# Kernel optimization log

Measured on AMD Instinct MI355X. Metric: run time of the kernel, lower is better.

Reference implementation:

```python
import jax, jax.numpy as jnp
import numpy as np

N_CLASSES = 18

def setup_inputs() -> dict:
    key = jax.random.key(0)
    k1, k2 = jax.random.split(key)
    B = 2_000_000
    output = jax.random.normal(k1, (B, N_CLASSES), dtype=jnp.float32)
    labels_soft = jax.random.uniform(k2, (B, N_CLASSES), dtype=jnp.float32)
    return {"output": output, "labels_soft": labels_soft}

def reference(output, labels_soft):
    # Original: sum over classes of mean_b( CE(output, cls) * labels_soft[:, cls] )
    # = mean over batch of sum_c( -log_softmax(output)[b, c] * labels_soft[b, c] )
    logp = jax.nn.log_softmax(output, axis=-1)          # [B, C]
    per_row = -jnp.sum(logp * labels_soft, axis=-1)     # [B]
    return jnp.mean(per_row)
```

## Files before the change

### kernel.cpp

```cpp
#include <hip/hip_runtime.h>

#define NCLS 18
#define TILE_ROWS 256
#define TILE_F2 (TILE_ROWS * NCLS / 2)
#define GRID_A 2048

__global__ __launch_bounds__(256) void ce_soft_kernel(
    const float2* __restrict__ logits2,
    const float2* __restrict__ labels2,
    float* __restrict__ partials,
    int B)
{
    __shared__ float2 sX[TILE_F2];
    __shared__ float2 sL[TILE_F2];

    const int t = threadIdx.x;
    const int nTiles = (B + TILE_ROWS - 1) / TILE_ROWS;

    float acc = 0.0f;
    for (int tile = blockIdx.x; tile < nTiles; tile += gridDim.x) {
        const int rowBase = tile * TILE_ROWS;
        const int rows = min(TILE_ROWS, B - rowBase);
        const int n2 = rows * (NCLS / 2);
        const size_t g2 = (size_t)rowBase * (NCLS / 2);

        for (int g = t; g < n2; g += 256) {
            sX[g] = logits2[g2 + g];
            sL[g] = labels2[g2 + g];
        }
        __syncthreads();

        if (t < rows) {
            const float2* xr = &sX[t * (NCLS / 2)];
            const float2* lr = &sL[t * (NCLS / 2)];
            float x[NCLS];
            #pragma unroll
            for (int j = 0; j < NCLS / 2; ++j) {
                float2 v = xr[j];
                x[2 * j] = v.x; x[2 * j + 1] = v.y;
            }
            float m = x[0];
            #pragma unroll
            for (int c = 1; c < NCLS; ++c) m = fmaxf(m, x[c]);

            float se = 0.0f, dot = 0.0f, sl = 0.0f;
            #pragma unroll
            for (int j = 0; j < NCLS / 2; ++j) {
                float2 w = lr[j];
                se += __expf(x[2 * j] - m) + __expf(x[2 * j + 1] - m);
                dot = fmaf(w.x, x[2 * j], dot);
                dot = fmaf(w.y, x[2 * j + 1], dot);
                sl += w.x + w.y;
            }
            float lse = m + __logf(se);
            acc = fmaf(sl, lse, acc - dot);
        }
        __syncthreads();
    }

    #pragma unroll
    for (int off = 32; off > 0; off >>= 1)
        acc += __shfl_down(acc, off, 64);

    __shared__ float wave_sums[4];
    const int lane = t & 63;
    const int wid  = t >> 6;
    if (lane == 0) wave_sums[wid] = acc;
    __syncthreads();
    if (t == 0)
        partials[blockIdx.x] = wave_sums[0] + wave_sums[1] + wave_sums[2] + wave_sums[3];
}

__global__ __launch_bounds__(256) void ce_reduce_kernel(
    const float* __restrict__ partials, float* __restrict__ out, int n, float invB)
{
    float acc = 0.0f;
    for (int i = threadIdx.x; i < n; i += 256) acc += partials[i];

    #pragma unroll
    for (int off = 32; off > 0; off >>= 1)
        acc += __shfl_down(acc, off, 64);

    __shared__ float wave_sums[4];
    const int lane = threadIdx.x & 63;
    const int wid  = threadIdx.x >> 6;
    if (lane == 0) wave_sums[wid] = acc;
    __syncthreads();
    if (threadIdx.x == 0)
        out[0] = (wave_sums[0] + wave_sums[1] + wave_sums[2] + wave_sums[3]) * invB;
}

extern "C" void kernel_launch(void* const* d_in, const int* in_sizes, int n_in,
                              void* d_out, int out_size, void* d_ws, size_t ws_size,
                              hipStream_t stream) {
    const float2* logits2 = (const float2*)d_in[0];
    const float2* labels2 = (const float2*)d_in[1];
    float* partials = (float*)d_ws;
    float* result = (float*)d_out;

    int B = in_sizes[0] / NCLS;

    ce_soft_kernel<<<GRID_A, 256, 0, stream>>>(logits2, labels2, partials, B);
    ce_reduce_kernel<<<1, 256, 0, stream>>>(partials, result, GRID_A, 1.0f / (float)B);
}
```

Baseline: 294.3 us.

## Stage tiles per wavefront with register-batched loads and no block barriers

Each wavefront now owns a private 64-row chunk in shared memory and issues all of its global loads into registers before writing them to LDS, instead of a strided block-wide copy loop bracketed by __syncthreads. This removes the block barriers and puts more loads in flight per thread, so each wave can overlap memory latency on its own. Rows past the last full chunk go through a separate direct-from-global loop. Within a wave the correctness relies on lockstep execution plus an explicit lgkmcnt wait rather than a barrier, and the fixed register arrays raise register pressure.

```diff
diff --git a/kernel.cpp b/kernel.cpp
--- a/kernel.cpp
+++ b/kernel.cpp
@@ -1,8 +1,10 @@
 #include <hip/hip_runtime.h>
 
 #define NCLS 18
-#define TILE_ROWS 256
-#define TILE_F2 (TILE_ROWS * NCLS / 2)
+#define F2R 9
+#define CROWS 64
+#define CF2 (CROWS * F2R)
+#define WPB 4
 #define GRID_A 2048
 
 __global__ __launch_bounds__(256) void ce_soft_kernel(
@@ -11,64 +13,81 @@
     float* __restrict__ partials,
     int B)
 {
-    __shared__ float2 sX[TILE_F2];
-    __shared__ float2 sL[TILE_F2];
+    __shared__ float2 sX[WPB][CF2];
+    __shared__ float2 sL[WPB][CF2];
 
-    const int t = threadIdx.x;
-    const int nTiles = (B + TILE_ROWS - 1) / TILE_ROWS;
+    const int t    = threadIdx.x;
+    const int lane = t & 63;
+    const int wid  = t >> 6;
+    const int gw   = blockIdx.x * WPB + wid;
+    const int nw   = gridDim.x * WPB;
+    const int nChunks = B / CROWS;
 
     float acc = 0.0f;
-    for (int tile = blockIdx.x; tile < nTiles; tile += gridDim.x) {
-        const int rowBase = tile * TILE_ROWS;
-        const int rows = min(TILE_ROWS, B - rowBase);
-        const int n2 = rows * (NCLS / 2);
-        const size_t g2 = (size_t)rowBase * (NCLS / 2);
 
-        for (int g = t; g < n2; g += 256) {
-            sX[g] = logits2[g2 + g];
-            sL[g] = labels2[g2 + g];
+    for (int ch = gw; ch < nChunks; ch += nw) {
+        const size_t g2 = (size_t)ch * CF2;
+
+        float2 vx[F2R], vl[F2R];
+        #pragma unroll
+        for (int j = 0; j < F2R; ++j) vx[j] = logits2[g2 + (size_t)(j * 64 + lane)];
+        #pragma unroll
+        for (int j = 0; j < F2R; ++j) vl[j] = labels2[g2 + (size_t)(j * 64 + lane)];
+
+        #pragma unroll
+        for (int j = 0; j < F2R; ++j) sX[wid][j * 64 + lane] = vx[j];
+        #pragma unroll
+        for (int j = 0; j < F2R; ++j) sL[wid][j * 64 + lane] = vl[j];
+
+        __asm__ volatile("s_waitcnt lgkmcnt(0)" ::: "memory");
+
+        const float2* xr = &sX[wid][lane * F2R];
+        const float2* lr = &sL[wid][lane * F2R];
+
+        float x[NCLS];
+        #pragma unroll
+        for (int j = 0; j < F2R; ++j) { float2 v = xr[j]; x[2*j] = v.x; x[2*j+1] = v.y; }
+
+        float m = x[0];
+        #pragma unroll
+        for (int c = 1; c < NCLS; ++c) m = fmaxf(m, x[c]);
+
+        float se = 0.0f, dot = 0.0f, sl = 0.0f;
+        #pragma unroll
+        for (int j = 0; j < F2R; ++j) {
+            float2 w = lr[j];
+            se += __expf(x[2*j] - m) + __expf(x[2*j+1] - m);
+            dot = fmaf(w.x, x[2*j], dot);
+            dot = fmaf(w.y, x[2*j+1], dot);
+            sl += w.x + w.y;
         }
-        __syncthreads();
+        acc = fmaf(sl, m + __logf(se), acc - dot);
+    }
 
-        if (t < rows) {
-            const float2* xr = &sX[t * (NCLS / 2)];
-            const float2* lr = &sL[t * (NCLS / 2)];
-            float x[NCLS];
-            #pragma unroll
-            for (int j = 0; j < NCLS / 2; ++j) {
-                float2 v = xr[j];
-                x[2 * j] = v.x; x[2 * j + 1] = v.y;
-            }
-            float m = x[0];
-            #pragma unroll
-            for (int c = 1; c < NCLS; ++c) m = fmaxf(m, x[c]);
-
-            float se = 0.0f, dot = 0.0f, sl = 0.0f;
-            #pragma unroll
-            for (int j = 0; j < NCLS / 2; ++j) {
-                float2 w = lr[j];
-                se += __expf(x[2 * j] - m) + __expf(x[2 * j + 1] - m);
-                dot = fmaf(w.x, x[2 * j], dot);
-                dot = fmaf(w.y, x[2 * j + 1], dot);
-                sl += w.x + w.y;
-            }
-            float lse = m + __logf(se);
-            acc = fmaf(sl, lse, acc - dot);
-        }
-        __syncthreads();
+    for (int row = nChunks * CROWS + gw * 64 + lane; row < B; row += nw * 64) {
+        const float2* o2 = logits2 + (size_t)row * F2R;
+        const float2* l2 = labels2 + (size_t)row * F2R;
+        float x[NCLS], l[NCLS];
+        #pragma unroll
+        for (int j = 0; j < F2R; ++j) { float2 v = o2[j]; x[2*j] = v.x; x[2*j+1] = v.y; }
+        #pragma unroll
+        for (int j = 0; j < F2R; ++j) { float2 w = l2[j]; l[2*j] = w.x; l[2*j+1] = w.y; }
+        float m = x[0];
+        #pragma unroll
+        for (int c = 1; c < NCLS; ++c) m = fmaxf(m, x[c]);
+        float se = 0.0f, dot = 0.0f, sl = 0.0f;
+        #pragma unroll
+        for (int c = 0; c < NCLS; ++c) { se += __expf(x[c] - m); dot = fmaf(l[c], x[c], dot); sl += l[c]; }
+        acc = fmaf(sl, m + __logf(se), acc - dot);
     }
 
     #pragma unroll
-    for (int off = 32; off > 0; off >>= 1)
-        acc += __shfl_down(acc, off, 64);
+    for (int off = 32; off > 0; off >>= 1) acc += __shfl_down(acc, off, 64);
 
-    __shared__ float wave_sums[4];
-    const int lane = t & 63;
-    const int wid  = t >> 6;
-    if (lane == 0) wave_sums[wid] = acc;
+    __shared__ float wsum[WPB];
+    if (lane == 0) wsum[wid] = acc;
     __syncthreads();
-    if (t == 0)
-        partials[blockIdx.x] = wave_sums[0] + wave_sums[1] + wave_sums[2] + wave_sums[3];
+    if (t == 0) partials[blockIdx.x] = wsum[0] + wsum[1] + wsum[2] + wsum[3];
 }
 
 __global__ __launch_bounds__(256) void ce_reduce_kernel(
@@ -78,8 +97,7 @@
     for (int i = threadIdx.x; i < n; i += 256) acc += partials[i];
 
     #pragma unroll
-    for (int off = 32; off > 0; off >>= 1)
-        acc += __shfl_down(acc, off, 64);
+    for (int off = 32; off > 0; off >>= 1) acc += __shfl_down(acc, off, 64);
 
     __shared__ float wave_sums[4];
     const int lane = threadIdx.x & 63;
```

Measured after the change: 295.0 us. Within noise of the previous version (+0.3%).
